# Kernel optimization log

Measured on AMD Instinct MI355X. Metric: run time of the kernel, lower is better.

The kernel has to match this reference:

```python
import jax, jax.numpy as jnp
import numpy as np

B, S, V, D, H, L, C = 64, 128, 50000, 300, 128, 20, 3
EPS = 1e-8


def lstm(x, w_ih, w_hh, b):
    # x: (B,S,D) -> outputs (B,S,H); torch gate order i,f,g,o
    xg = jnp.einsum('bsd,gd->bsg', x, w_ih) + b  # (B,S,4H)
    Hh = w_hh.shape[1]

    def step(carry, xt):
        hprev, cprev = carry
        g = xt + hprev @ w_hh.T
        i, f, gg, o = jnp.split(g, 4, axis=-1)
        c = jax.nn.sigmoid(f) * cprev + jax.nn.sigmoid(i) * jnp.tanh(gg)
        hnew = jax.nn.sigmoid(o) * jnp.tanh(c)
        return (hnew, c), hnew

    z = jnp.zeros((x.shape[0], Hh), x.dtype)
    _, hs = jax.lax.scan(step, (z, z), xg.transpose(1, 0, 2))
    return hs.transpose(1, 0, 2)


def bilstm(x, wih_f, whh_f, b_f, wih_b, whh_b, b_b):
    fwd = lstm(x, wih_f, whh_f, b_f)
    bwd = jnp.flip(lstm(jnp.flip(x, 1), wih_b, whh_b, b_b), 1)
    return jnp.concatenate([fwd, bwd], axis=-1)


def safe_div(prod, norm):
    # matches module's cosine_similarity eps handling
    return prod / jnp.where(norm > EPS, norm, EPS)


def full_matching(p1, p2, w):
    # p1: (B,S,H), p2: (B,H), w: (H,L) -> (B,S,L)
    v1 = p1[:, :, :, None] * w          # (B,S,H,L)
    v2 = p2[:, :, None] * w             # (B,H,L)
    dot = jnp.einsum('bshl,bhl->bsl', v1, v2)
    n1 = jnp.linalg.norm(v1, axis=2)    # (B,S,L)
    n2 = jnp.linalg.norm(v2, axis=1)    # (B,L)
    return dot / (jnp.maximum(n1, EPS) * jnp.maximum(n2, EPS)[:, None, :])


def maxpool_matching(p1, p2, w):
    v1 = p1[..., None] * w              # (B,S,H,L)
    v2 = p2[..., None] * w              # (B,T,H,L)
    prod = jnp.einsum('bshl,bthl->blst', v1, v2)
    n1 = jnp.linalg.norm(v1, axis=2)    # (B,S,L)
    n2 = jnp.linalg.norm(v2, axis=2)    # (B,T,L)
    deno = jnp.einsum('bsl,btl->blst', n1, n2)
    return safe_div(prod, deno).max(axis=3).transpose(0, 2, 1)  # (B,S,L)


def _wcos(a, b, w):
    # F.cosine_similarity over hidden dim of a*w vs b*w -> (B,S,L)
    va = a[..., None] * w
    vb = b[..., None] * w
    dot = jnp.einsum('bshl,bshl->bsl', va, vb)
    na = jnp.linalg.norm(va, axis=2)
    nb = jnp.linalg.norm(vb, axis=2)
    return dot / (jnp.maximum(na, EPS) * jnp.maximum(nb, EPS))


def attentive_matching(p1, p2, w_att, w_max):
    n1 = jnp.linalg.norm(p1, axis=2, keepdims=True)   # (B,S,1)
    n2 = jnp.linalg.norm(p2, axis=2, keepdims=True)   # (B,T,1)
    alpha = safe_div(jnp.einsum('bsh,bth->bst', p1, p2),
                     n1 * n2.transpose(0, 2, 1))       # (B,S,T)
    max_idx = jnp.argmax(alpha, axis=2)                # (B,S)
    h_mat = jnp.einsum('bst,bth->bsh', alpha, p2)
    resultant = h_mat / alpha.sum(axis=2, keepdims=True)
    result_match = _wcos(resultant, p1, w_att)
    out_mat = jnp.take_along_axis(p2, max_idx[..., None], axis=1)  # (B,S,H)
    result_max = _wcos(out_mat, p1, w_max)
    return result_match, result_max


def setup_inputs() -> dict:
    key = jax.random.key(0)
    ks = jax.random.split(key, 32)
    g = lambda k, shp, s=0.05: (jax.random.normal(k, shp, jnp.float32) * s)
    inp = {
        'emb': g(ks[0], (V, D), 0.1),
        'ctx_wih_f': g(ks[1], (4 * H, D)), 'ctx_whh_f': g(ks[2], (4 * H, H)), 'ctx_b_f': jnp.zeros((4 * H,), jnp.float32),
        'ctx_wih_b': g(ks[3], (4 * H, D)), 'ctx_whh_b': g(ks[4], (4 * H, H)), 'ctx_b_b': jnp.zeros((4 * H,), jnp.float32),
        'agg_wih_f': g(ks[5], (4 * H, 8 * L)), 'agg_whh_f': g(ks[6], (4 * H, H)), 'agg_b_f': jnp.zeros((4 * H,), jnp.float32),
        'agg_wih_b': g(ks[7], (4 * H, 8 * L)), 'agg_whh_b': g(ks[8], (4 * H, H)), 'agg_b_b': jnp.zeros((4 * H,), jnp.float32),
        'pW1': g(ks[9], (2 * H, 4 * H)), 'pb1': jnp.zeros((2 * H,), jnp.float32),
        'pW2': g(ks[10], (C, 2 * H)), 'pb2': jnp.zeros((C,), jnp.float32),
        'p': jax.random.randint(ks[11], (B, S), 0, V),
        'h': jax.random.randint(ks[12], (B, S), 0, V),
    }
    for i in range(1, 9):
        inp[f'w{i}'] = g(ks[12 + i], (H, L), 0.5)
    return inp


def reference(emb, ctx_wih_f, ctx_whh_f, ctx_b_f, ctx_wih_b, ctx_whh_b, ctx_b_b,
              agg_wih_f, agg_whh_f, agg_b_f, agg_wih_b, agg_whh_b, agg_b_b,
              pW1, pb1, pW2, pb2, w1, w2, w3, w4, w5, w6, w7, w8, p, h):
    p1_in = emb[p]
    p2_in = emb[h]
    c1 = bilstm(p1_in, ctx_wih_f, ctx_whh_f, ctx_b_f, ctx_wih_b, ctx_whh_b, ctx_b_b)
    c2 = bilstm(p2_in, ctx_wih_f, ctx_whh_f, ctx_b_f, ctx_wih_b, ctx_whh_b, ctx_b_b)
    c1f, c1b = jnp.split(c1, 2, axis=-1)
    c2f, c2b = jnp.split(c2, 2, axis=-1)

    match_p1_f = full_matching(c1f, c2f[:, -1], w1)
    match_p1_b = full_matching(c1b, c2b[:, -1], w2)
    match_p2_f = full_matching(c2f, c1f[:, -1], w1)
    match_p2_b = full_matching(c2b, c1b[:, -1], w2)

    maxm_p1_f = maxpool_matching(c1f, c2f, w3)
    maxm_p1_b = maxpool_matching(c1b, c2b, w4)
    maxm_p2_f = maxpool_matching(c2f, c1f, w3)
    maxm_p2_b = maxpool_matching(c2b, c1b, w4)

    att_p1_f, attm_p1_f = attentive_matching(c1f, c2f, w5, w7)
    att_p1_b, attm_p1_b = attentive_matching(c1b, c2b, w6, w8)
    att_p2_f, attm_p2_f = attentive_matching(c2f, c1f, w5, w7)
    att_p2_b, attm_p2_b = attentive_matching(c2b, c1b, w6, w8)

    aggr_p1 = jnp.concatenate([match_p1_f, match_p1_b, maxm_p1_f, maxm_p1_b,
                               att_p1_f, att_p1_b, attm_p1_f, attm_p1_b], axis=2)
    aggr_p2 = jnp.concatenate([match_p2_f, match_p2_b, maxm_p2_f, maxm_p2_b,
                               att_p2_f, att_p2_b, attm_p2_f, attm_p2_b], axis=2)

    agg_p = bilstm(aggr_p1, agg_wih_f, agg_whh_f, agg_b_f, agg_wih_b, agg_whh_b, agg_b_b)
    agg_h = bilstm(aggr_p2, agg_wih_f, agg_whh_f, agg_b_f, agg_wih_b, agg_whh_b, agg_b_b)
    out = jnp.concatenate([agg_p[:, -1], agg_h[:, -1]], axis=1)  # (B,4H)
    out = jax.nn.relu(out @ pW1.T + pb1) @ pW2.T + pb2
    return out
```

## Files before the change

kernel.cpp:

```cpp
#include <hip/hip_runtime.h>
#include <math.h>

#define B_  64
#define S_  128
#define H_  128
#define D_  300
#define L_  20
#define G4  512
#define SH  (S_*H_)
#define BSH ((size_t)B_*SH)
#define EPSV 1e-8f

typedef __attribute__((ext_vector_type(8))) short bshort8;
typedef __attribute__((ext_vector_type(4))) float f32x4;

__device__ __forceinline__ unsigned fmap(float f){
  unsigned u = __float_as_uint(f);
  return (u & 0x80000000u) ? ~u : (u | 0x80000000u);
}
__device__ __forceinline__ float funmap(unsigned u){
  return __uint_as_float((u & 0x80000000u) ? (u & 0x7fffffffu) : ~u);
}
__device__ __forceinline__ float sigmf(float x){ return 1.f/(1.f+expf(-x)); }
__device__ __forceinline__ float dot4(float4 a, float4 b){
  return a.x*b.x + a.y*b.y + a.z*b.z + a.w*b.w;
}
__device__ __forceinline__ float blane(float v, int k){
  return __int_as_float(__builtin_amdgcn_readlane(__float_as_int(v), k));
}
__device__ __forceinline__ unsigned short f2bf(float f){
  unsigned u = __float_as_uint(f);
  unsigned r = u + 0x7fffu + ((u >> 16) & 1u);
  return (unsigned short)(r >> 16);
}
__device__ __forceinline__ float bf2f(unsigned short us){
  return __uint_as_float(((unsigned)us) << 16);
}
__device__ __forceinline__ int swz64(int row, int h){
  return (row << 6) + ((((h >> 2) ^ ((row >> 3) & 15)) << 2) | (h & 3));
}
__device__ __forceinline__ int swz128(int row, int h){
  return (row << 7) + ((((h >> 2) ^ ((row >> 3) & 15)) << 2) | (h & 3));
}
__device__ __forceinline__ int bswz(int row, int slot){
  return (row << 7) + (((slot ^ (row & 15)) << 3));
}
__device__ __forceinline__ void cvt8(float4 a0, float4 a1, int4& hi, int4& lo){
  float v[8] = {a0.x, a0.y, a0.z, a0.w, a1.x, a1.y, a1.z, a1.w};
  unsigned short h[8], l[8];
  #pragma unroll
  for (int i = 0; i < 8; i++) {
    h[i] = f2bf(v[i]);
    float d = v[i] - bf2f(h[i]);
    l[i] = f2bf(d);
  }
  hi = make_int4((unsigned)h[0] | ((unsigned)h[1] << 16), (unsigned)h[2] | ((unsigned)h[3] << 16),
                 (unsigned)h[4] | ((unsigned)h[5] << 16), (unsigned)h[6] | ((unsigned)h[7] << 16));
  lo = make_int4((unsigned)l[0] | ((unsigned)l[1] << 16), (unsigned)l[2] | ((unsigned)l[3] << 16),
                 (unsigned)l[4] | ((unsigned)l[5] << 16), (unsigned)l[6] | ((unsigned)l[7] << 16));
}

__global__ void k_embed(const float* __restrict__ emb, const int* __restrict__ p,
                        const int* __restrict__ h, float* __restrict__ x1,
                        float* __restrict__ x2)
{
  int row = blockIdx.x;
  const int* idx = blockIdx.y ? h : p;
  float* x = blockIdx.y ? x2 : x1;
  int tok = idx[row];
  const float* src = emb + (size_t)tok * D_;
  float* dst = x + (size_t)row * D_;
  for (int d = threadIdx.x; d < D_; d += blockDim.x) dst[d] = src[d];
}

template<int K>
__global__ __launch_bounds__(512, 1) void gemm_abt(
    const float* __restrict__ A0, const float* __restrict__ A1,
    const float* __restrict__ W0, const float* __restrict__ W1,
    const float* __restrict__ b0, const float* __restrict__ b1,
    float* __restrict__ Cbase, int M, int N)
{
  int q = blockIdx.z;
  const float* A = (q >> 1) ? A1 : A0;
  const float* W = (q & 1) ? W1 : W0;
  const float* bias = (q & 1) ? b1 : b0;
  float* Cm = Cbase + (size_t)q * M * N;

  __shared__ __align__(16) short AsH[128 * 32];
  __shared__ __align__(16) short AsL[128 * 32];
  __shared__ __align__(16) short WsH[128 * 32];
  __shared__ __align__(16) short WsL[128 * 32];

  int t = threadIdx.x;
  int w = t >> 6, lane = t & 63;
  int r = lane & 15, g = lane >> 4;
  int m0 = blockIdx.x * 128, n0 = blockIdx.y * 128;
  int mbase = (w & 1) * 64;
  int nbase = (w >> 1) * 32;

  f32x4 acc[4][2];
  #pragma unroll
  for (int i = 0; i < 4; i++)
    #pragma unroll
    for (int j = 0; j < 2; j++) acc[i][j] = (f32x4){0.f, 0.f, 0.f, 0.f};

  int srow = t >> 2, skc = t & 3;
  int soff = srow * 32 + ((skc ^ ((srow >> 1) & 3)) << 3);

  #pragma unroll 1
  for (int k0 = 0; k0 < K; k0 += 32) {
    {
      int gk = k0 + (skc << 3);
      float4 z = make_float4(0.f, 0.f, 0.f, 0.f);
      float4 a0v = z, a1v = z, w0v = z, w1v = z;
      if (gk < K) {
        a0v = *(const float4*)&A[(size_t)(m0 + srow) * K + gk];
        w0v = *(const float4*)&W[(size_t)(n0 + srow) * K + gk];
      }
      if (gk + 4 < K) {
        a1v = *(const float4*)&A[(size_t)(m0 + srow) * K + gk + 4];
        w1v = *(const float4*)&W[(size_t)(n0 + srow) * K + gk + 4];
      }
      int4 hi, lo;
      cvt8(a0v, a1v, hi, lo);
      *(int4*)&AsH[soff] = hi; *(int4*)&AsL[soff] = lo;
      cvt8(w0v, w1v, hi, lo);
      *(int4*)&WsH[soff] = hi; *(int4*)&WsL[soff] = lo;
    }
    __syncthreads();
    bshort8 ah[4], al[4], bh[2], bl[2];
    #pragma unroll
    for (int i = 0; i < 4; i++) {
      int R = mbase + i * 16 + r;
      int off = R * 32 + ((g ^ ((R >> 1) & 3)) << 3);
      ah[i] = *(const bshort8*)&AsH[off];
      al[i] = *(const bshort8*)&AsL[off];
    }
    #pragma unroll
    for (int j = 0; j < 2; j++) {
      int R = nbase + j * 16 + r;
      int off = R * 32 + ((g ^ ((R >> 1) & 3)) << 3);
      bh[j] = *(const bshort8*)&WsH[off];
      bl[j] = *(const bshort8*)&WsL[off];
    }
    #pragma unroll
    for (int i = 0; i < 4; i++)
      #pragma unroll
      for (int j = 0; j < 2; j++) {
        acc[i][j] = __builtin_amdgcn_mfma_f32_16x16x32_bf16(ah[i], bh[j], acc[i][j], 0, 0, 0);
        acc[i][j] = __builtin_amdgcn_mfma_f32_16x16x32_bf16(ah[i], bl[j], acc[i][j], 0, 0, 0);
        acc[i][j] = __builtin_amdgcn_mfma_f32_16x16x32_bf16(al[i], bh[j], acc[i][j], 0, 0, 0);
      }
    __syncthreads();
  }
  #pragma unroll
  for (int j = 0; j < 2; j++) {
    int gcol = n0 + nbase + j * 16 + r;
    float bv = bias[gcol];
    #pragma unroll
    for (int i = 0; i < 4; i++) {
      #pragma unroll
      for (int rg = 0; rg < 4; rg++) {
        int grow = m0 + mbase + i * 16 + g * 4 + rg;
        Cm[(size_t)grow * N + gcol] = acc[i][j][rg] + bv;
      }
    }
  }
}

__global__ __launch_bounds__(512, 1) void k_lstm(const float* __restrict__ xg,
    const float* __restrict__ whhF, const float* __restrict__ whhB,
    float* __restrict__ hs)
{
  int b = blockIdx.x, q = blockIdx.y, dir = q & 1;
  const float* whh = dir ? whhB : whhF;
  const float* xgq = xg + ((size_t)(q * B_ + b)) * (S_ * G4);
  float* out = hs + ((size_t)(q * B_ + b)) * SH;
  int j = threadIdx.x;
  int lane = j & 63;

  float w[128];
  #pragma unroll
  for (int k = 0; k < 128; k += 4) {
    float4 v = *(const float4*)(whh + (size_t)j * 128 + k);
    w[k] = v.x; w[k + 1] = v.y; w[k + 2] = v.z; w[k + 3] = v.w;
  }
  __shared__ float hsm[128];
  __shared__ float csm[128];
  __shared__ float gsm[512];
  if (j < 128) { hsm[j] = 0.f; csm[j] = 0.f; }
  __syncthreads();

  float h0 = 0.f, h1 = 0.f;
  float xnext = xgq[(size_t)(dir ? (S_ - 1) : 0) * G4 + j];

  for (int st = 0; st < S_; st++) {
    int tt = dir ? (S_ - 1 - st) : st;
    float xcur = xnext;
    {
      int stn = (st + 1 < S_) ? st + 1 : st;
      int ttn = dir ? (S_ - 1 - stn) : stn;
      xnext = xgq[(size_t)ttn * G4 + j];
    }
    float a0 = xcur, a1 = 0.f, a2 = 0.f, a3 = 0.f;
    #pragma unroll
    for (int k = 0; k < 64; k += 4) {
      a0 += w[k]     * blane(h0, k);
      a1 += w[k + 1] * blane(h0, k + 1);
      a2 += w[k + 2] * blane(h0, k + 2);
      a3 += w[k + 3] * blane(h0, k + 3);
    }
    #pragma unroll
    for (int k = 0; k < 64; k += 4) {
      a0 += w[64 + k]     * blane(h1, k);
      a1 += w[64 + k + 1] * blane(h1, k + 1);
      a2 += w[64 + k + 2] * blane(h1, k + 2);
      a3 += w[64 + k + 3] * blane(h1, k + 3);
    }
    gsm[j] = (a0 + a1) + (a2 + a3);
    __syncthreads();
    if (j < 128) {
      float ig = sigmf(gsm[j]);
      float fg = sigmf(gsm[128 + j]);
      float gg = tanhf(gsm[256 + j]);
      float og = sigmf(gsm[384 + j]);
      float c = fg * csm[j] + ig * gg;
      float hn = og * tanhf(c);
      csm[j] = c; hsm[j] = hn;
      out[(size_t)tt * H_ + j] = hn;
    }
    __syncthreads();
    h0 = hsm[lane];
    h1 = hsm[64 + lane];
  }
}

__global__ __launch_bounds__(256) void k_full(const float* __restrict__ C,
    const float* __restrict__ w1, const float* __restrict__ w2,
    float* __restrict__ ag1, float* __restrict__ ag2)
{
  int b = blockIdx.x, q = blockIdx.y, dir = q & 1;
  const float* p1  = C + (size_t)q * BSH + (size_t)b * SH;
  const float* p2l = C + (size_t)((q + 2) & 3) * BSH + (size_t)b * SH + (size_t)(S_ - 1) * H_;
  const float* w = dir ? w2 : w1;
  float* out = (q < 2 ? ag1 : ag2) + (size_t)b * S_ * 160;

  __shared__ float p1s[SH];
  __shared__ float ws2[H_][L_];
  __shared__ float p2s[H_];
  __shared__ float n2s[L_];
  int t = threadIdx.x;
  for (int i = t; i < SH; i += 256) p1s[i] = p1[i];
  for (int i = t; i < H_ * L_; i += 256) { float v = w[i]; ws2[i / L_][i % L_] = v * v; }
  if (t < H_) p2s[t] = p2l[t];
  __syncthreads();
  if (t < L_) {
    float s = 0.f;
    for (int hh = 0; hh < H_; hh++) { float v = p2s[hh]; s += v * v * ws2[hh][t]; }
    n2s[t] = sqrtf(s);
  }
  __syncthreads();
  for (int i = t; i < S_ * L_; i += 256) {
    int s = i / L_, l = i % L_;
    const float* pr = p1s + s * H_;
    float dot = 0.f, n1 = 0.f;
    for (int hh = 0; hh < H_; hh++) {
      float a = pr[hh], ww = ws2[hh][l];
      dot += a * p2s[hh] * ww;
      n1 += a * a * ww;
    }
    n1 = sqrtf(n1);
    out[(size_t)s * 160 + dir * L_ + l] = dot / (fmaxf(n1, EPSV) * fmaxf(n2s[l], EPSV));
  }
}

__global__ __launch_bounds__(512, 1) void k_maxpool(const float* __restrict__ C,
    const float* __restrict__ w3, const float* __restrict__ w4,
    float* __restrict__ ag1, float* __restrict__ ag2)
{
  int b = blockIdx.x, dir = blockIdx.y, lh = blockIdx.z;
  const float* p1 = C + (size_t)(0 + dir) * BSH + (size_t)b * SH;
  const float* p2 = C + (size_t)(2 + dir) * BSH + (size_t)b * SH;
  const float* w = dir ? w4 : w3;

  __shared__ __align__(16) short P1b[128 * 128];
  __shared__ __align__(16) short P2b[128 * 128];
  __shared__ __align__(16) short Ab[128 * 128];
  __shared__ float w2s[128 * 10];
  __shared__ float n1s[128], n2s[128];
  __shared__ unsigned mx2u[128];

  int t = threadIdx.x;
  int wv = t >> 6, lane = t & 63;
  int g = lane >> 4, col = lane & 15;

  for (int i = t; i < 8192; i += 512) {
    int row = i >> 6, hp = i & 63;
    int phys = bswz(row, hp >> 2) + ((hp & 3) << 1);
    float2 v1 = *(const float2*)&p1[(row << 7) + (hp << 1)];
    float2 v2 = *(const float2*)&p2[(row << 7) + (hp << 1)];
    *(unsigned*)&P1b[phys] = (unsigned)f2bf(v1.x) | ((unsigned)f2bf(v1.y) << 16);
    *(unsigned*)&P2b[phys] = (unsigned)f2bf(v2.x) | ((unsigned)f2bf(v2.y) << 16);
  }
  for (int i = t; i < 128 * 10; i += 512) {
    int hh = i / 10, lq = i % 10;
    float wv_ = w[hh * L_ + lh * 10 + lq];
    w2s[i] = wv_ * wv_;
  }
  __syncthreads();

  #pragma unroll 1
  for (int lq = 0; lq < 10; lq++) {
    int lout = lh * 10 + lq;
    for (int i = t; i < 8192; i += 512) {
      int row = i >> 6, hp = i & 63;
      int phys = bswz(row, hp >> 2) + ((hp & 3) << 1);
      unsigned u = *(const unsigned*)&P1b[phys];
      float lo = bf2f((unsigned short)(u & 0xffffu)) * w2s[(hp << 1) * 10 + lq];
      float hi = bf2f((unsigned short)(u >> 16))     * w2s[((hp << 1) + 1) * 10 + lq];
      *(unsigned*)&Ab[phys] = (unsigned)f2bf(lo) | ((unsigned)f2bf(hi) << 16);
    }
    {
      int s = t >> 2, part = t & 3;
      float s1 = 0.f, s2 = 0.f;
      #pragma unroll 1
      for (int hp = part * 16; hp < part * 16 + 16; hp++) {
        int phys = bswz(s, hp >> 2) + ((hp & 3) << 1);
        unsigned u1 = *(const unsigned*)&P1b[phys];
        unsigned u2 = *(const unsigned*)&P2b[phys];
        float wlo = w2s[(hp << 1) * 10 + lq];
        float whi = w2s[((hp << 1) + 1) * 10 + lq];
        float a = bf2f((unsigned short)(u1 & 0xffffu)), bb = bf2f((unsigned short)(u1 >> 16));
        float c2 = bf2f((unsigned short)(u2 & 0xffffu)), d2 = bf2f((unsigned short)(u2 >> 16));
        s1 += a * a * wlo + bb * bb * whi;
        s2 += c2 * c2 * wlo + d2 * d2 * whi;
      }
      s1 += __shfl_xor(s1, 1, 64); s1 += __shfl_xor(s1, 2, 64);
      s2 += __shfl_xor(s2, 1, 64); s2 += __shfl_xor(s2, 2, 64);
      if (part == 0) { n1s[s] = sqrtf(s1); n2s[s] = sqrtf(s2); }
    }
    if (t < 128) mx2u[t] = fmap(-3.4e38f);
    __syncthreads();

    {
      int mrow = (wv << 4) + col;
      f32x4 acc0 = {0,0,0,0}, acc1 = {0,0,0,0}, acc2 = {0,0,0,0}, acc3 = {0,0,0,0};
      f32x4 acc4 = {0,0,0,0}, acc5 = {0,0,0,0}, acc6 = {0,0,0,0}, acc7 = {0,0,0,0};
      #pragma unroll 1
      for (int k0 = 0; k0 < 128; k0 += 32) {
        int slot = ((k0 >> 3) + g) ^ col;
        bshort8 av = *(const bshort8*)&Ab[(mrow << 7) + (slot << 3)];
        bshort8 bv0 = *(const bshort8*)&P2b[((0 << 4) + col << 7) + (slot << 3)];
        bshort8 bv1 = *(const bshort8*)&P2b[(((1 << 4) + col) << 7) + (slot << 3)];
        bshort8 bv2 = *(const bshort8*)&P2b[(((2 << 4) + col) << 7) + (slot << 3)];
        bshort8 bv3 = *(const bshort8*)&P2b[(((3 << 4) + col) << 7) + (slot << 3)];
        bshort8 bv4 = *(const bshort8*)&P2b[(((4 << 4) + col) << 7) + (slot << 3)];
        bshort8 bv5 = *(const bshort8*)&P2b[(((5 << 4) + col) << 7) + (slot << 3)];
        bshort8 bv6 = *(const bshort8*)&P2b[(((6 << 4) + col) << 7) + (slot << 3)];
        bshort8 bv7 = *(const bshort8*)&P2b[(((7 << 4) + col) << 7) + (slot << 3)];
        acc0 = __builtin_amdgcn_mfma_f32_16x16x32_bf16(av, bv0, acc0, 0, 0, 0);
        acc1 = __builtin_amdgcn_mfma_f32_16x16x32_bf16(av, bv1, acc1, 0, 0, 0);
        acc2 = __builtin_amdgcn_mfma_f32_16x16x32_bf16(av, bv2, acc2, 0, 0, 0);
        acc3 = __builtin_amdgcn_mfma_f32_16x16x32_bf16(av, bv3, acc3, 0, 0, 0);
        acc4 = __builtin_amdgcn_mfma_f32_16x16x32_bf16(av, bv4, acc4, 0, 0, 0);
        acc5 = __builtin_amdgcn_mfma_f32_16x16x32_bf16(av, bv5, acc5, 0, 0, 0);
        acc6 = __builtin_amdgcn_mfma_f32_16x16x32_bf16(av, bv6, acc6, 0, 0, 0);
        acc7 = __builtin_amdgcn_mfma_f32_16x16x32_bf16(av, bv7, acc7, 0, 0, 0);
      }
      float n1v[4];
      #pragma unroll
      for (int r = 0; r < 4; r++) n1v[r] = n1s[(wv << 4) + (g << 2) + r];
      float rm[4] = {-3.4e38f, -3.4e38f, -3.4e38f, -3.4e38f};
      float cm[8];
      f32x4 accs[8] = {acc0, acc1, acc2, acc3, acc4, acc5, acc6, acc7};
      #pragma unroll
      for (int c = 0; c < 8; c++) {
        float n2v = n2s[(c << 4) + col];
        float cmx = -3.4e38f;
        #pragma unroll
        for (int r = 0; r < 4; r++) {
          float deno = n1v[r] * n2v;
          float cs = accs[c][r] / (deno > EPSV ? deno : EPSV);
          rm[r] = fmaxf(rm[r], cs);
          cmx = fmaxf(cmx, cs);
        }
        cm[c] = cmx;
      }
      #pragma unroll
      for (int m = 1; m < 16; m <<= 1)
        #pragma unroll
        for (int r = 0; r < 4; r++) rm[r] = fmaxf(rm[r], __shfl_xor(rm[r], m, 64));
      if (col == 0) {
        #pragma unroll
        for (int r = 0; r < 4; r++) {
          int srow = (wv << 4) + (g << 2) + r;
          ag1[(size_t)b * S_ * 160 + (size_t)srow * 160 + 40 + dir * L_ + lout] = rm[r];
        }
      }
      #pragma unroll
      for (int c = 0; c < 8; c++) {
        cm[c] = fmaxf(cm[c], __shfl_xor(cm[c], 16, 64));
        cm[c] = fmaxf(cm[c], __shfl_xor(cm[c], 32, 64));
      }
      if (lane < 16) {
        #pragma unroll
        for (int c = 0; c < 8; c++) atomicMax(&mx2u[(c << 4) + lane], fmap(cm[c]));
      }
    }
    __syncthreads();
    if (t < 128)
      ag2[(size_t)b * S_ * 160 + (size_t)t * 160 + 40 + dir * L_ + lout] = funmap(mx2u[t]);
    __syncthreads();
  }
}

__global__ __launch_bounds__(256, 1) void k_alpha(const float* __restrict__ C,
                                                  float* __restrict__ alpha)
{
  int b = blockIdx.x, dir = blockIdx.y;
  const float* p1 = C + (size_t)(0 + dir) * BSH + (size_t)b * SH;
  const float* p2 = C + (size_t)(2 + dir) * BSH + (size_t)b * SH;
  __shared__ __align__(16) float a1[128 * 64];
  __shared__ __align__(16) float a2[128 * 64];
  __shared__ float n1p[128], n2p[128];
  int t = threadIdx.x, tx = t & 15, ty = t >> 4;
  float acc[8][8] = {};

  for (int pass = 0; pass < 2; pass++) {
    int h0 = pass << 6;
    for (int i = t; i < 128 * 64; i += 256) {
      int row = i >> 6, hh = i & 63;
      int off = swz64(row, hh);
      a1[off] = p1[(size_t)row * H_ + h0 + hh];
      a2[off] = p2[(size_t)row * H_ + h0 + hh];
    }
    __syncthreads();
    {
      int r = t & 127;
      const float* a = (t < 128) ? a1 : a2;
      float s = 0.f;
      #pragma unroll 1
      for (int f = 0; f < 16; f++) {
        float4 v = *(const float4*)&a[(r << 6) + ((f ^ ((r >> 3) & 15)) << 2)];
        s += dot4(v, v);
      }
      float* np = (t < 128) ? n1p : n2p;
      if (pass == 0) np[r] = s; else np[r] += s;
    }
    #pragma unroll 1
    for (int f = 0; f < 16; f++) {
      int cx = ((f ^ ty) << 2);
      int cy = ((f ^ tx) << 2);
      float4 x[8], y[8];
      #pragma unroll
      for (int i = 0; i < 8; i++) x[i] = *(const float4*)&a1[((8 * ty + i) << 6) + cx];
      #pragma unroll
      for (int j = 0; j < 8; j++) y[j] = *(const float4*)&a2[((8 * tx + j) << 6) + cy];
      #pragma unroll
      for (int i = 0; i < 8; i++)
        #pragma unroll
        for (int j = 0; j < 8; j++) acc[i][j] += dot4(x[i], y[j]);
    }
    __syncthreads();
  }
  float inv1[8], inv2[8];
  #pragma unroll
  for (int i = 0; i < 8; i++) inv1[i] = 1.f / fmaxf(sqrtf(n1p[8 * ty + i]), EPSV);
  #pragma unroll
  for (int j = 0; j < 8; j++) inv2[j] = 1.f / fmaxf(sqrtf(n2p[8 * tx + j]), EPSV);
  float* outp = alpha + ((size_t)dir * B_ + b) * SH;
  #pragma unroll
  for (int i = 0; i < 8; i++) {
    int ss = 8 * ty + i;
    float s1 = inv1[i];
    float4 o0 = make_float4(acc[i][0] * s1 * inv2[0], acc[i][1] * s1 * inv2[1],
                            acc[i][2] * s1 * inv2[2], acc[i][3] * s1 * inv2[3]);
    float4 o1 = make_float4(acc[i][4] * s1 * inv2[4], acc[i][5] * s1 * inv2[5],
                            acc[i][6] * s1 * inv2[6], acc[i][7] * s1 * inv2[7]);
    *(float4*)&outp[(size_t)ss * S_ + 8 * tx] = o0;
    *(float4*)&outp[(size_t)ss * S_ + 8 * tx + 4] = o1;
  }
}

__global__ __launch_bounds__(256, 1) void k_att(const float* __restrict__ C,
    const float* __restrict__ alpha,
    const float* __restrict__ w5, const float* __restrict__ w6,
    const float* __restrict__ w7, const float* __restrict__ w8,
    float* __restrict__ ag1, float* __restrict__ ag2)
{
  int b = blockIdx.x, q = blockIdx.y, dir = q & 1;
  const float* p1  = C + (size_t)q * BSH + (size_t)b * SH;
  const float* m2g = C + (size_t)((q + 2) & 3) * BSH + (size_t)b * SH;
  const float* wa = dir ? w6 : w5;
  const float* wm = dir ? w8 : w7;
  const float* ain = alpha + ((size_t)dir * B_ + b) * SH;
  float* out = (q < 2 ? ag1 : ag2) + (size_t)b * S_ * 160;
  bool tr = (q >= 2);

  __shared__ __align__(16) float A[128 * 128];
  __shared__ __align__(16) float M2T[128 * 128];
  __shared__ __align__(16) float waT[20 * 128];
  __shared__ __align__(16) float wmT[20 * 128];
  __shared__ float rowsum[128];
  __shared__ int   midx[128];
  int t = threadIdx.x, tx = t & 15, ty = t >> 4;

  for (int i = t; i < SH; i += 256) {
    int r = i >> 7, c = i & 127;
    float av = ain[i];
    if (tr) A[swz128(c, r)] = av; else A[swz128(r, c)] = av;
    M2T[swz128(c, r)] = m2g[i];
  }
  for (int i = t; i < H_ * L_; i += 256) {
    int hh = i / L_, l = i % L_;
    float v = wa[i]; waT[l * 128 + hh] = v * v;
    float u = wm[i]; wmT[l * 128 + hh] = u * u;
  }
  __syncthreads();

  if (t < 128) {
    float sum = 0.f, best = -3.4e38f; int bi = 0;
    #pragma unroll 1
    for (int f = 0; f < 32; f++) {
      float4 v = *(const float4*)&A[(t << 7) + (((f ^ ((t >> 3) & 15)) & 31) << 2)];
      sum += v.x + v.y + v.z + v.w;
      int k = f << 2;
      if (v.x > best) { best = v.x; bi = k; }
      if (v.y > best) { best = v.y; bi = k + 1; }
      if (v.z > best) { best = v.z; bi = k + 2; }
      if (v.w > best) { best = v.w; bi = k + 3; }
    }
    rowsum[t] = sum; midx[t] = bi;
  }
  __syncthreads();

  float acc[8][8] = {};
  #pragma unroll 1
  for (int f = 0; f < 32; f++) {
    int cx = (((f ^ ty) & 31) << 2);
    int cy = (((f ^ tx) & 31) << 2);
    float4 x[8], y[8];
    #pragma unroll
    for (int i = 0; i < 8; i++) x[i] = *(const float4*)&A[((8 * ty + i) << 7) + cx];
    #pragma unroll
    for (int j = 0; j < 8; j++) y[j] = *(const float4*)&M2T[((8 * tx + j) << 7) + cy];
    #pragma unroll
    for (int i = 0; i < 8; i++)
      #pragma unroll
      for (int j = 0; j < 8; j++) acc[i][j] += dot4(x[i], y[j]);
  }
  __syncthreads();
  {
    float rinv[8];
    #pragma unroll
    for (int i = 0; i < 8; i++) rinv[i] = 1.f / rowsum[8 * ty + i];
    #pragma unroll
    for (int i = 0; i < 8; i++) {
      int row = 8 * ty + i;
      int f0 = (2 * tx) ^ ((row >> 3) & 15);
      int f1 = (2 * tx + 1) ^ ((row >> 3) & 15);
      float4 o0 = make_float4(acc[i][0] * rinv[i], acc[i][1] * rinv[i],
                              acc[i][2] * rinv[i], acc[i][3] * rinv[i]);
      float4 o1 = make_float4(acc[i][4] * rinv[i], acc[i][5] * rinv[i],
                              acc[i][6] * rinv[i], acc[i][7] * rinv[i]);
      *(float4*)&A[(row << 7) + (f0 << 2)] = o0;
      *(float4*)&A[(row << 7) + (f1 << 2)] = o1;
    }
  }
  __syncthreads();

  {
    int s = t >> 1, l0 = (t & 1) * 10;
    int mi = midx[s];
    const float* m2r = m2g + (size_t)mi * H_;
    const float* p1r = p1 + (size_t)s * H_;
    float dA[10] = {}, nA[10] = {}, bA[10] = {};
    float dM[10] = {}, nM[10] = {}, bM[10] = {};
    #pragma unroll 1
    for (int f = 0; f < 32; f++) {
      float4 pv = *(const float4*)&p1r[f << 2];
      float4 mv = *(const float4*)&m2r[f << 2];
      float4 av = *(const float4*)&A[(s << 7) + (((f ^ ((s >> 3) & 15)) & 31) << 2)];
      float4 ap = make_float4(av.x*pv.x, av.y*pv.y, av.z*pv.z, av.w*pv.w);
      float4 a2 = make_float4(av.x*av.x, av.y*av.y, av.z*av.z, av.w*av.w);
      float4 p2 = make_float4(pv.x*pv.x, pv.y*pv.y, pv.z*pv.z, pv.w*pv.w);
      float4 mp = make_float4(mv.x*pv.x, mv.y*pv.y, mv.z*pv.z, mv.w*pv.w);
      float4 m2 = make_float4(mv.x*mv.x, mv.y*mv.y, mv.z*mv.z, mv.w*mv.w);
      #pragma unroll
      for (int l = 0; l < 10; l++) {
        float4 wv = *(const float4*)&waT[(l0 + l) * 128 + (f << 2)];
        dA[l] += dot4(ap, wv); nA[l] += dot4(a2, wv); bA[l] += dot4(p2, wv);
        float4 uv = *(const float4*)&wmT[(l0 + l) * 128 + (f << 2)];
        dM[l] += dot4(mp, uv); nM[l] += dot4(m2, uv); bM[l] += dot4(p2, uv);
      }
    }
    #pragma unroll
    for (int l = 0; l < 10; l++) {
      int ll = l0 + l;
      out[(size_t)s * 160 + 80  + dir * L_ + ll] =
          dA[l] / (fmaxf(sqrtf(nA[l]), EPSV) * fmaxf(sqrtf(bA[l]), EPSV));
      out[(size_t)s * 160 + 120 + dir * L_ + ll] =
          dM[l] / (fmaxf(sqrtf(nM[l]), EPSV) * fmaxf(sqrtf(bM[l]), EPSV));
    }
  }
}

__global__ __launch_bounds__(256) void k_final(const float* __restrict__ Cc,
    const float* __restrict__ pW1, const float* __restrict__ pb1,
    const float* __restrict__ pW2, const float* __restrict__ pb2,
    float* __restrict__ out)
{
  int b = blockIdx.x, t = threadIdx.x;
  __shared__ float cat[512];
  __shared__ float hid[256];
  if (t < 128) {
    cat[t]       = Cc[(size_t)(0 * B_ + b) * SH + (size_t)(S_ - 1) * H_ + t];
    cat[128 + t] = Cc[(size_t)(1 * B_ + b) * SH + (size_t)(S_ - 1) * H_ + t];
    cat[256 + t] = Cc[(size_t)(2 * B_ + b) * SH + (size_t)(S_ - 1) * H_ + t];
    cat[384 + t] = Cc[(size_t)(3 * B_ + b) * SH + (size_t)(S_ - 1) * H_ + t];
  }
  __syncthreads();
  float a = pb1[t];
  for (int k = 0; k < 512; k++) a += cat[k] * pW1[(size_t)t * 512 + k];
  hid[t] = fmaxf(a, 0.f);
  __syncthreads();
  if (t < 3) {
    float o = pb2[t];
    for (int k = 0; k < 256; k++) o += hid[k] * pW2[(size_t)t * 256 + k];
    out[(size_t)b * 3 + t] = o;
  }
}

extern "C" void kernel_launch(void* const* d_in, const int* in_sizes, int n_in,
                              void* d_out, int out_size, void* d_ws, size_t ws_size,
                              hipStream_t stream)
{
  const float* emb    = (const float*)d_in[0];
  const float* cwih_f = (const float*)d_in[1];
  const float* cwhh_f = (const float*)d_in[2];
  const float* cb_f   = (const float*)d_in[3];
  const float* cwih_b = (const float*)d_in[4];
  const float* cwhh_b = (const float*)d_in[5];
  const float* cb_b   = (const float*)d_in[6];
  const float* awih_f = (const float*)d_in[7];
  const float* awhh_f = (const float*)d_in[8];
  const float* ab_f   = (const float*)d_in[9];
  const float* awih_b = (const float*)d_in[10];
  const float* awhh_b = (const float*)d_in[11];
  const float* ab_b   = (const float*)d_in[12];
  const float* pW1    = (const float*)d_in[13];
  const float* pb1    = (const float*)d_in[14];
  const float* pW2    = (const float*)d_in[15];
  const float* pb2    = (const float*)d_in[16];
  const int*   pidx   = (const int*)d_in[17];
  const int*   hidx   = (const int*)d_in[18];
  const float* w1 = (const float*)d_in[19];
  const float* w2 = (const float*)d_in[20];
  const float* w3 = (const float*)d_in[21];
  const float* w4 = (const float*)d_in[22];
  const float* w5 = (const float*)d_in[23];
  const float* w6 = (const float*)d_in[24];
  const float* w7 = (const float*)d_in[25];
  const float* w8 = (const float*)d_in[26];

  float* ws = (float*)d_ws;
  float* XG   = ws;
  float* X1   = ws + 16777216;
  float* X2   = X1 + 2457600;
  float* ALPH = X1;
  float* AG1  = ws + 16777216 + 2097152;
  float* AG2  = AG1 + (size_t)B_ * S_ * 160;
  float* CC   = ws + 21692416;

  k_embed<<<dim3(B_ * S_, 2), 256, 0, stream>>>(emb, pidx, hidx, X1, X2);
  gemm_abt<D_><<<dim3(64, 4, 4), 512, 0, stream>>>(X1, X2, cwih_f, cwih_b, cb_f, cb_b,
                                                   XG, B_ * S_, G4);
  k_lstm<<<dim3(B_, 4), 512, 0, stream>>>(XG, cwhh_f, cwhh_b, CC);
  k_full<<<dim3(B_, 4), 256, 0, stream>>>(CC, w1, w2, AG1, AG2);
  k_maxpool<<<dim3(B_, 2, 2), 512, 0, stream>>>(CC, w3, w4, AG1, AG2);
  k_alpha<<<dim3(B_, 2), 256, 0, stream>>>(CC, ALPH);
  k_att<<<dim3(B_, 4), 256, 0, stream>>>(CC, ALPH, w5, w6, w7, w8, AG1, AG2);
  gemm_abt<8 * L_><<<dim3(64, 4, 4), 512, 0, stream>>>(AG1, AG2, awih_f, awih_b, ab_f, ab_b,
                                                       XG, B_ * S_, G4);
  k_lstm<<<dim3(B_, 4), 512, 0, stream>>>(XG, awhh_f, awhh_b, CC);
  k_final<<<dim3(B_), 256, 0, stream>>>(CC, pW1, pb1, pW2, pb2, (float*)d_out);
}
```

Baseline: 659.0 us.

## Batch LSTM recurrence across 16 sequences per block using split-bf16 MFMA

The recurrent step now processes 16 batch rows per block. It computes h·Whh^T with bf16 hi/lo split MFMA, with the weights held in registers and h double-buffered in shared memory, in place of per-sequence scalar dot products built on readlane. The input-projection GEMM permutes its output columns so each lane's four gates are contiguous, which lets the gate math run in registers with one barrier per step. Fast exp-based sigmoid and tanh replace the library calls. This cuts the LSTM grid from 256 to 16 blocks, trading parallelism for far less per-step work, and it introduces small precision differences.

```diff
diff --git a/kernel.cpp b/kernel.cpp
--- a/kernel.cpp
+++ b/kernel.cpp
@@ -22,11 +22,10 @@
   return __uint_as_float((u & 0x80000000u) ? (u & 0x7fffffffu) : ~u);
 }
 __device__ __forceinline__ float sigmf(float x){ return 1.f/(1.f+expf(-x)); }
+__device__ __forceinline__ float fsigm(float x){ return 1.f/(1.f+__expf(-x)); }
+__device__ __forceinline__ float ftanh(float x){ return 1.f - 2.f/(__expf(2.f*x)+1.f); }
 __device__ __forceinline__ float dot4(float4 a, float4 b){
   return a.x*b.x + a.y*b.y + a.z*b.z + a.w*b.w;
-}
-__device__ __forceinline__ float blane(float v, int k){
-  return __int_as_float(__builtin_amdgcn_readlane(__float_as_int(v), k));
 }
 __device__ __forceinline__ unsigned short f2bf(float f){
   unsigned u = __float_as_uint(f);
@@ -73,7 +72,7 @@
   for (int d = threadIdx.x; d < D_; d += blockDim.x) dst[d] = src[d];
 }
 
-template<int K>
+template<int K, bool PERM>
 __global__ __launch_bounds__(512, 1) void gemm_abt(
     const float* __restrict__ A0, const float* __restrict__ A1,
     const float* __restrict__ W0, const float* __restrict__ W1,
@@ -106,6 +105,8 @@
 
   int srow = t >> 2, skc = t & 3;
   int soff = srow * 32 + ((skc ^ ((srow >> 1) & 3)) << 3);
+  int nrow = n0 + srow;
+  int wrow = PERM ? ((nrow & 3) * 128 + (nrow >> 2)) : nrow;
 
   #pragma unroll 1
   for (int k0 = 0; k0 < K; k0 += 32) {
@@ -115,11 +116,11 @@
       float4 a0v = z, a1v = z, w0v = z, w1v = z;
       if (gk < K) {
         a0v = *(const float4*)&A[(size_t)(m0 + srow) * K + gk];
-        w0v = *(const float4*)&W[(size_t)(n0 + srow) * K + gk];
+        w0v = *(const float4*)&W[(size_t)wrow * K + gk];
       }
       if (gk + 4 < K) {
         a1v = *(const float4*)&A[(size_t)(m0 + srow) * K + gk + 4];
-        w1v = *(const float4*)&W[(size_t)(n0 + srow) * K + gk + 4];
+        w1v = *(const float4*)&W[(size_t)wrow * K + gk + 4];
       }
       int4 hi, lo;
       cvt8(a0v, a1v, hi, lo);
@@ -156,7 +157,7 @@
   #pragma unroll
   for (int j = 0; j < 2; j++) {
     int gcol = n0 + nbase + j * 16 + r;
-    float bv = bias[gcol];
+    float bv = bias[PERM ? ((gcol & 3) * 128 + (gcol >> 2)) : gcol];
     #pragma unroll
     for (int i = 0; i < 4; i++) {
       #pragma unroll
@@ -172,66 +173,103 @@
     const float* __restrict__ whhF, const float* __restrict__ whhB,
     float* __restrict__ hs)
 {
-  int b = blockIdx.x, q = blockIdx.y, dir = q & 1;
+  int bt = blockIdx.x, q = blockIdx.y, dir = q & 1;
   const float* whh = dir ? whhB : whhF;
-  const float* xgq = xg + ((size_t)(q * B_ + b)) * (S_ * G4);
-  float* out = hs + ((size_t)(q * B_ + b)) * SH;
-  int j = threadIdx.x;
-  int lane = j & 63;
-
-  float w[128];
+  int t = threadIdx.x;
+  int w = t >> 6, lane = t & 63;
+  int r15 = lane & 15, g4 = lane >> 4;
+  int bcol = r15;
+  int bglob = bt * 16 + bcol;
+  const float* xgq = xg + ((size_t)(q * B_ + bglob)) * (S_ * G4);
+  float* outb = hs + ((size_t)(q * B_ + bglob)) * SH;
+
+  bshort8 ahi[4][4], alo[4][4];
   #pragma unroll
-  for (int k = 0; k < 128; k += 4) {
-    float4 v = *(const float4*)(whh + (size_t)j * 128 + k);
-    w[k] = v.x; w[k + 1] = v.y; w[k + 2] = v.z; w[k + 3] = v.w;
-  }
-  __shared__ float hsm[128];
-  __shared__ float csm[128];
-  __shared__ float gsm[512];
-  if (j < 128) { hsm[j] = 0.f; csm[j] = 0.f; }
-  __syncthreads();
-
-  float h0 = 0.f, h1 = 0.f;
-  float xnext = xgq[(size_t)(dir ? (S_ - 1) : 0) * G4 + j];
-
+  for (int i = 0; i < 4; i++) {
+    int mt = w * 4 + i;
+    int grow = (r15 & 3) * 128 + mt * 4 + (r15 >> 2);
+    #pragma unroll
+    for (int ks = 0; ks < 4; ks++) {
+      int k0 = ks * 32 + g4 * 8;
+      float4 v0 = *(const float4*)&whh[(size_t)grow * 128 + k0];
+      float4 v1 = *(const float4*)&whh[(size_t)grow * 128 + k0 + 4];
+      int4 hi, lo;
+      cvt8(v0, v1, hi, lo);
+      ahi[i][ks] = *(bshort8*)&hi;
+      alo[i][ks] = *(bshort8*)&lo;
+    }
+  }
+
+  __shared__ unsigned Hu[2 * 16 * 140];
+  for (int i = t; i < 2 * 16 * 140; i += 512) Hu[i] = 0u;
+  float creg[4] = {0.f, 0.f, 0.f, 0.f};
+  __syncthreads();
+
+  float4 xcur[4], xnxt[4];
+  {
+    int tt0 = dir ? (S_ - 1) : 0;
+    #pragma unroll
+    for (int i = 0; i < 4; i++)
+      xnxt[i] = *(const float4*)&xgq[(size_t)tt0 * G4 + 16 * (w * 4 + i) + 4 * g4];
+  }
+
+  #pragma unroll 1
   for (int st = 0; st < S_; st++) {
     int tt = dir ? (S_ - 1 - st) : st;
-    float xcur = xnext;
+    int cur = st & 1, nxt = cur ^ 1;
+    #pragma unroll
+    for (int i = 0; i < 4; i++) xcur[i] = xnxt[i];
     {
       int stn = (st + 1 < S_) ? st + 1 : st;
       int ttn = dir ? (S_ - 1 - stn) : stn;
-      xnext = xgq[(size_t)ttn * G4 + j];
-    }
-    float a0 = xcur, a1 = 0.f, a2 = 0.f, a3 = 0.f;
-    #pragma unroll
-    for (int k = 0; k < 64; k += 4) {
-      a0 += w[k]     * blane(h0, k);
-      a1 += w[k + 1] * blane(h0, k + 1);
-      a2 += w[k + 2] * blane(h0, k + 2);
-      a3 += w[k + 3] * blane(h0, k + 3);
-    }
-    #pragma unroll
-    for (int k = 0; k < 64; k += 4) {
-      a0 += w[64 + k]     * blane(h1, k);
-      a1 += w[64 + k + 1] * blane(h1, k + 1);
-      a2 += w[64 + k + 2] * blane(h1, k + 2);
-      a3 += w[64 + k + 3] * blane(h1, k + 3);
-    }
-    gsm[j] = (a0 + a1) + (a2 + a3);
+      #pragma unroll
+      for (int i = 0; i < 4; i++)
+        xnxt[i] = *(const float4*)&xgq[(size_t)ttn * G4 + 16 * (w * 4 + i) + 4 * g4];
+    }
+    f32x4 acc[4];
+    #pragma unroll
+    for (int i = 0; i < 4; i++) acc[i] = (f32x4){0.f, 0.f, 0.f, 0.f};
+    #pragma unroll
+    for (int ks = 0; ks < 4; ks++) {
+      int k0 = ks * 32 + g4 * 8;
+      int base = cur * 2240 + bcol * 140 + k0;
+      int4 p0 = *(const int4*)&Hu[base];
+      int4 p1 = *(const int4*)&Hu[base + 4];
+      int4 hi4, lo4;
+      hi4.x = (p0.x & 0xffff) | (p0.y << 16);
+      hi4.y = (p0.z & 0xffff) | (p0.w << 16);
+      hi4.z = (p1.x & 0xffff) | (p1.y << 16);
+      hi4.w = (p1.z & 0xffff) | (p1.w << 16);
+      lo4.x = (int)(((unsigned)p0.x >> 16) | ((unsigned)p0.y & 0xffff0000u));
+      lo4.y = (int)(((unsigned)p0.z >> 16) | ((unsigned)p0.w & 0xffff0000u));
+      lo4.z = (int)(((unsigned)p1.x >> 16) | ((unsigned)p1.y & 0xffff0000u));
+      lo4.w = (int)(((unsigned)p1.z >> 16) | ((unsigned)p1.w & 0xffff0000u));
+      bshort8 bhi = *(bshort8*)&hi4;
+      bshort8 blo = *(bshort8*)&lo4;
+      #pragma unroll
+      for (int i = 0; i < 4; i++) {
+        acc[i] = __builtin_amdgcn_mfma_f32_16x16x32_bf16(ahi[i][ks], bhi, acc[i], 0, 0, 0);
+        acc[i] = __builtin_amdgcn_mfma_f32_16x16x32_bf16(ahi[i][ks], blo, acc[i], 0, 0, 0);
+        acc[i] = __builtin_amdgcn_mfma_f32_16x16x32_bf16(alo[i][ks], bhi, acc[i], 0, 0, 0);
+      }
+    }
+    #pragma unroll
+    for (int i = 0; i < 4; i++) {
+      int hidx = (w * 4 + i) * 4 + g4;
+      float gi = acc[i][0] + xcur[i].x;
+      float gf = acc[i][1] + xcur[i].y;
+      float gg = acc[i][2] + xcur[i].z;
+      float go = acc[i][3] + xcur[i].w;
+      float ig = fsigm(gi), fg = fsigm(gf);
+      float gv = ftanh(gg), og = fsigm(go);
+      creg[i] = fg * creg[i] + ig * gv;
+      float hn = og * ftanh(creg[i]);
+      outb[(size_t)tt * H_ + hidx] = hn;
+      unsigned short hhi = f2bf(hn);
+      unsigned short hlo = f2bf(hn - bf2f(hhi));
+      Hu[nxt * 2240 + bcol * 140 + hidx] = (unsigned)hhi | ((unsigned)hlo << 16);
+    }
     __syncthreads();
-    if (j < 128) {
-      float ig = sigmf(gsm[j]);
-      float fg = sigmf(gsm[128 + j]);
-      float gg = tanhf(gsm[256 + j]);
-      float og = sigmf(gsm[384 + j]);
-      float c = fg * csm[j] + ig * gg;
-      float hn = og * tanhf(c);
-      csm[j] = c; hsm[j] = hn;
-      out[(size_t)tt * H_ + j] = hn;
-    }
-    __syncthreads();
-    h0 = hsm[lane];
-    h1 = hsm[64 + lane];
   }
 }
 
@@ -673,15 +711,15 @@
   float* CC   = ws + 21692416;
 
   k_embed<<<dim3(B_ * S_, 2), 256, 0, stream>>>(emb, pidx, hidx, X1, X2);
-  gemm_abt<D_><<<dim3(64, 4, 4), 512, 0, stream>>>(X1, X2, cwih_f, cwih_b, cb_f, cb_b,
-                                                   XG, B_ * S_, G4);
-  k_lstm<<<dim3(B_, 4), 512, 0, stream>>>(XG, cwhh_f, cwhh_b, CC);
+  gemm_abt<D_, true><<<dim3(64, 4, 4), 512, 0, stream>>>(X1, X2, cwih_f, cwih_b, cb_f, cb_b,
+                                                         XG, B_ * S_, G4);
+  k_lstm<<<dim3(B_ / 16, 4), 512, 0, stream>>>(XG, cwhh_f, cwhh_b, CC);
   k_full<<<dim3(B_, 4), 256, 0, stream>>>(CC, w1, w2, AG1, AG2);
   k_maxpool<<<dim3(B_, 2, 2), 512, 0, stream>>>(CC, w3, w4, AG1, AG2);
   k_alpha<<<dim3(B_, 2), 256, 0, stream>>>(CC, ALPH);
   k_att<<<dim3(B_, 4), 256, 0, stream>>>(CC, ALPH, w5, w6, w7, w8, AG1, AG2);
-  gemm_abt<8 * L_><<<dim3(64, 4, 4), 512, 0, stream>>>(AG1, AG2, awih_f, awih_b, ab_f, ab_b,
-                                                       XG, B_ * S_, G4);
-  k_lstm<<<dim3(B_, 4), 512, 0, stream>>>(XG, awhh_f, awhh_b, CC);
+  gemm_abt<8 * L_, true><<<dim3(64, 4, 4), 512, 0, stream>>>(AG1, AG2, awih_f, awih_b, ab_f, ab_b,
+                                                             XG, B_ * S_, G4);
+  k_lstm<<<dim3(B_ / 16, 4), 512, 0, stream>>>(XG, awhh_f, awhh_b, CC);
   k_final<<<dim3(B_), 256, 0, stream>>>(CC, pW1, pb1, pW2, pb2, (float*)d_out);
 }
```

After: 916.8 us. 1.39x slower.
